# Kernel tuning notes

Measured on AMD Instinct MI355X. Metric: run time of the kernel, lower is better.

## Reference

```python
import jax, jax.numpy as jnp
import numpy as np

H = 64          # HIDDEN_DIM
V = 64          # VOCAB_SIZE
LN_EPS = 1e-5   # torch LayerNorm default
D_EPS = 1e-6    # denom epsilon in delta rule
MEM_SCALE = 1.0 # forward default arg


def setup_inputs() -> dict:
    key = jax.random.key(0)
    ks = jax.random.split(key, 8)
    B, L = 16, 2048
    s = lambda k, shape: (jax.random.normal(k, shape, jnp.float32) * 0.05)
    return {
        "seq": jax.random.randint(ks[0], (B, L), 0, V),
        "embed": s(ks[1], (V, H)),
        "W1": s(ks[2], (H, 2 * H)), "b1": jnp.zeros((2 * H,), jnp.float32),
        "W2": s(ks[3], (2 * H, H)), "b2": jnp.zeros((H,), jnp.float32),
        "gamma": jnp.ones((H,), jnp.float32), "beta": jnp.zeros((H,), jnp.float32),
        "Wr": s(ks[4], (H, H)), "br": jnp.zeros((H,), jnp.float32),
        "Wo": s(ks[5], (H, V)), "bo": jnp.zeros((V,), jnp.float32),
    }


def reference(seq, embed, W1, b1, W2, b2, gamma, beta, Wr, br, Wo, bo):
    h = embed[seq]                                  # (B, L, H)
    ff = jax.nn.relu(h @ W1 + b1) @ W2 + b2         # (B, L, H)
    x = h + ff
    mu = x.mean(-1, keepdims=True)
    var = x.var(-1, keepdims=True)                  # biased, as torch LayerNorm
    h = (x - mu) / jnp.sqrt(var + LN_EPS) * gamma + beta

    B = h.shape[0]
    keys = jnp.swapaxes(h[:, :-1, :], 0, 1)         # (L-1, B, H): all but last token

    def step(M, k):                                  # M: (B, H, H), k: (B, H)
        v_pred = jnp.einsum('bij,bj->bi', M, k)
        denom = (k * k).sum(-1, keepdims=True) + D_EPS
        dv = k - v_pred / denom
        M = M + MEM_SCALE * dv[:, :, None] * k[:, None, :]
        return M, None

    M0 = jnp.zeros((B, H, H), h.dtype)
    M, _ = jax.lax.scan(step, M0, keys)

    q = h[:, -1, :]                                  # last token as query
    ctx = jnp.einsum('bij,bj->bi', M, q)             # (B, H)
    return (ctx @ Wr + br) @ Wo + bo                 # (B, V)
```

## Files before the change

### kernel.cpp

```cpp
#include <hip/hip_runtime.h>

#define HDIM 64
#define LSEQ 2048
#define BATCH 16
#define LN_EPS 1e-5f
#define D_EPS 1e-6f
#define NSEG 32
#define CPS 4

typedef unsigned short u16;
typedef unsigned int   u32;
typedef __attribute__((ext_vector_type(8))) short bf16x8;
typedef __attribute__((ext_vector_type(4))) float f32x4;

__device__ __forceinline__ float bf2f(u16 v) {
    return __uint_as_float(((u32)v) << 16);
}
__device__ __forceinline__ u16 f2bf(float f) {
    u32 u = __float_as_uint(f);
    return (u16)((u + 0x7FFFu + ((u >> 16) & 1u)) >> 16);
}

#define A_W1F  0
#define A_W2F  16384
#define A_ER   32768
#define A_HF   50176
#define H_ROWS 66560
#define H_INVD 75264
#define SMEM_BYTES 75520
#define B_GM 0
#define B_BH 4352
#define B_BL 13568
#define B_SH 22784
#define B_SL 32000
#define B_ZN 41216
#define B_ZV 46336

__global__ __launch_bounds__(256, 2) void fused_pc_kernel(
    const int* __restrict__ seq, const float* __restrict__ embed,
    const float* __restrict__ W1, const float* __restrict__ b1,
    const float* __restrict__ W2, const float* __restrict__ b2,
    const float* __restrict__ gamma, const float* __restrict__ beta,
    u32* __restrict__ PK, u16* __restrict__ q_ws)
{
    __shared__ __align__(16) char smem[SMEM_BYTES];
    const int t = threadIdx.x;
    const int b = blockIdx.x >> 5;
    const int s = blockIdx.x & 31;
    const int tok0 = 1984 - 64 * s;

    u16*   hrows  = (u16*)(smem + H_ROWS);
    float* invd_l = (float*)(smem + H_INVD);

    const int lane = t & 63;
    const int w    = t >> 6;
    const int g    = lane >> 4;
    const int c    = lane & 15;

    {
        u16*   sW1f = (u16*)(smem + A_W1F);
        u16*   sW2f = (u16*)(smem + A_W2F);
        float* eR   = (float*)(smem + A_ER);
        u16*   hF   = (u16*)(smem + A_HF);

        {
            const float4* s1 = (const float4*)W1;
#pragma unroll
            for (int q = 0; q < 8; ++q) {
                const int m = t + 256 * q;
                const int k = m >> 5;
                const int o0 = (m & 31) * 4;
                const float4 v = s1[m];
                const float e4[4] = {v.x, v.y, v.z, v.w};
                const int ks = k >> 5, l4 = ((k >> 3) & 3) << 4, i = k & 7;
#pragma unroll
                for (int e = 0; e < 4; ++e) {
                    const int o = o0 + e;
                    sW1f[((ks * 8 + (o >> 4)) * 64 + l4 + (o & 15)) * 8 + i] = f2bf(e4[e]);
                }
            }
            const float4* s2 = (const float4*)W2;
#pragma unroll
            for (int q = 0; q < 8; ++q) {
                const int m = t + 256 * q;
                const int k = m >> 4;
                const int o0 = (m & 15) * 4;
                const float4 v = s2[m];
                const float e4[4] = {v.x, v.y, v.z, v.w};
                const int ks = k >> 5, l4 = ((k >> 3) & 3) << 4, i = k & 7;
#pragma unroll
                for (int e = 0; e < 4; ++e) {
                    const int o = o0 + e;
                    sW2f[((ks * 4 + (o >> 4)) * 64 + l4 + (o & 15)) * 8 + i] = f2bf(e4[e]);
                }
            }
        }
        {
            const int tk = t >> 2, p = t & 3;
            const int v = seq[b * LSEQ + tok0 + tk];
            const float* er = embed + v * HDIM + 16 * p;
#pragma unroll
            for (int q = 0; q < 4; ++q)
                *(float4*)&eR[tk * 68 + 16 * p + 4 * q] = *(const float4*)(er + 4 * q);
        }
        __syncthreads();

        bf16x8 ea[2];
#pragma unroll
        for (int ks = 0; ks < 2; ++ks) {
            const float* src = &eR[(16 * w + c) * 68 + ks * 32 + g * 8];
            const float4 v0 = *(const float4*)src;
            const float4 v1 = *(const float4*)(src + 4);
            bf16x8 f;
            f[0] = (short)f2bf(v0.x); f[1] = (short)f2bf(v0.y);
            f[2] = (short)f2bf(v0.z); f[3] = (short)f2bf(v0.w);
            f[4] = (short)f2bf(v1.x); f[5] = (short)f2bf(v1.y);
            f[6] = (short)f2bf(v1.z); f[7] = (short)f2bf(v1.w);
            ea[ks] = f;
        }

#pragma unroll
        for (int nt = 0; nt < 8; ++nt) {
            const float bv = b1[16 * nt + c];
            f32x4 acc = {bv, bv, bv, bv};
#pragma unroll
            for (int ks = 0; ks < 2; ++ks) {
                const bf16x8 bf = *(const bf16x8*)&sW1f[((ks * 8 + nt) * 64 + lane) * 8];
                acc = __builtin_amdgcn_mfma_f32_16x16x32_bf16(ea[ks], bf, acc, 0, 0, 0);
            }
            const int o   = 16 * nt + c;
            const int ks2 = o >> 5;
            const int l4  = ((o >> 3) & 3) << 4;
            const int i   = o & 7;
#pragma unroll
            for (int r = 0; r < 4; ++r) {
                const float hv = fmaxf(acc[r], 0.f);
                hF[((w * 4 + ks2) * 64 + l4 + g * 4 + r) * 8 + i] = f2bf(hv);
            }
        }

        bf16x8 ha[4];
#pragma unroll
        for (int ks = 0; ks < 4; ++ks)
            ha[ks] = *(const bf16x8*)&hF[((w * 4 + ks) * 64 + lane) * 8];

        float xf[4][4];
#pragma unroll
        for (int nt = 0; nt < 4; ++nt) {
            const float bv = b2[16 * nt + c];
            f32x4 acc = {bv, bv, bv, bv};
#pragma unroll
            for (int ks = 0; ks < 4; ++ks) {
                const bf16x8 bf = *(const bf16x8*)&sW2f[((ks * 4 + nt) * 64 + lane) * 8];
                acc = __builtin_amdgcn_mfma_f32_16x16x32_bf16(ha[ks], bf, acc, 0, 0, 0);
            }
#pragma unroll
            for (int r = 0; r < 4; ++r)
                xf[nt][r] = acc[r] + eR[(16 * w + g * 4 + r) * 68 + 16 * nt + c];
        }

        float s4[4] = {0, 0, 0, 0}, q4[4] = {0, 0, 0, 0};
#pragma unroll
        for (int nt = 0; nt < 4; ++nt)
#pragma unroll
            for (int r = 0; r < 4; ++r) {
                s4[r] += xf[nt][r];
                q4[r] = fmaf(xf[nt][r], xf[nt][r], q4[r]);
            }
#pragma unroll
        for (int m = 1; m < 16; m <<= 1)
#pragma unroll
            for (int r = 0; r < 4; ++r) {
                s4[r] += __shfl_xor(s4[r], m);
                q4[r] += __shfl_xor(q4[r], m);
            }
        float mu[4], rstd[4];
#pragma unroll
        for (int r = 0; r < 4; ++r) {
            mu[r] = s4[r] * (1.0f / 64.0f);
            const float var = q4[r] * (1.0f / 64.0f) - mu[r] * mu[r];
            rstd[r] = 1.0f / sqrtf(var + LN_EPS);
        }

        float hh[4] = {0, 0, 0, 0};
#pragma unroll
        for (int nt = 0; nt < 4; ++nt) {
            const int o = 16 * nt + c;
            const float gm = gamma[o], bt = beta[o];
#pragma unroll
            for (int r = 0; r < 4; ++r) {
                const float ov = (xf[nt][r] - mu[r]) * rstd[r] * gm + bt;
                const u16 rb = f2bf(ov);
                const float qf = bf2f(rb);
                hh[r] = fmaf(qf, qf, hh[r]);
                u16 st = rb;
                if (s == 0 && w == 3 && g == 3 && r == 3) {
                    q_ws[b * 64 + o] = rb;
                    st = 0;
                }
                hrows[(16 * w + g * 4 + r) * 68 + o] = st;
            }
        }
#pragma unroll
        for (int m = 1; m < 16; m <<= 1)
#pragma unroll
            for (int r = 0; r < 4; ++r) hh[r] += __shfl_xor(hh[r], m);
        if (c == 0) {
#pragma unroll
            for (int r = 0; r < 4; ++r)
                invd_l[16 * w + g * 4 + r] = 1.0f / (hh[r] + D_EPS);
        }
    }
    __syncthreads();

    {
        float* Gm = (float*)(smem + B_GM) + w * 272;
        u16*   Bh = (u16*)(smem + B_BH) + w * 1152;
        u16*   Bl = (u16*)(smem + B_BL) + w * 1152;
        u16*   Sh = (u16*)(smem + B_SH) + w * 1152;
        u16*   Sl = (u16*)(smem + B_SL) + w * 1152;
        u32*   Zn = (u32*)(smem + B_ZN) + w * 320;
        u32*   Zv = (u32*)(smem + B_ZV) + w * 320;

        f32x4 Sacc[4], Vacc[4];
#pragma unroll
        for (int mt = 0; mt < 4; ++mt) {
            ushort4 h4, l4;
            u16* hp = (u16*)&h4;
#pragma unroll
            for (int r = 0; r < 4; ++r) {
                const int m = 16 * mt + 4 * g + r;
                const float v = (m == 16 * w + c) ? 1.0f : 0.0f;
                Sacc[mt][r] = v;
                Vacc[mt][r] = 0.f;
                hp[r] = f2bf(v);
            }
            l4.x = 0; l4.y = 0; l4.z = 0; l4.w = 0;
            *(ushort4*)&Sh[c * 72 + 16 * mt + 4 * g] = h4;
            *(ushort4*)&Sl[c * 72 + 16 * mt + 4 * g] = l4;
        }

        for (int cc = 0; cc < CPS; ++cc) {
            const int base = 63 - 16 * cc;

            bf16x8 ka[2];
#pragma unroll
            for (int f = 0; f < 2; ++f) {
                const u16* src = &hrows[(base - c) * 68 + f * 32 + g * 8];
                const ushort4 a0 = *(const ushort4*)src;
                const ushort4 a1 = *(const ushort4*)(src + 4);
                bf16x8 kf;
                kf[0] = (short)a0.x; kf[1] = (short)a0.y; kf[2] = (short)a0.z; kf[3] = (short)a0.w;
                kf[4] = (short)a1.x; kf[5] = (short)a1.y; kf[6] = (short)a1.z; kf[7] = (short)a1.w;
                ka[f] = kf;
            }
            f32x4 gacc = {0.f, 0.f, 0.f, 0.f};
            gacc = __builtin_amdgcn_mfma_f32_16x16x32_bf16(ka[0], ka[0], gacc, 0, 0, 0);
            gacc = __builtin_amdgcn_mfma_f32_16x16x32_bf16(ka[1], ka[1], gacc, 0, 0, 0);
            const float ivc = invd_l[base - c];
#pragma unroll
            for (int r = 0; r < 4; ++r)
                Gm[(4 * g + r) * 17 + c] = gacc[r] * ivc;

            float Breg[16];
#pragma unroll
            for (int i = 0; i < 16; ++i) {
                float acc = bf2f(hrows[(base - i) * 68 + lane]);
#pragma unroll
                for (int j = 0; j < 16; ++j)
                    if (j < i) acc = fmaf(-Gm[i * 17 + j], Breg[j], acc);
                Breg[i] = acc;
            }
#pragma unroll
            for (int i = 0; i < 16; ++i) {
                const u16 hb = f2bf(Breg[i]);
                const u16 lb = f2bf(Breg[i] - bf2f(hb));
                Bh[i * 72 + lane] = hb;
                Bl[i * 72 + lane] = lb;
            }

            const bf16x8 abh0 = *(const bf16x8*)&Bh[c * 72 +  0 + g * 8];
            const bf16x8 abh1 = *(const bf16x8*)&Bh[c * 72 + 32 + g * 8];
            const bf16x8 abl0 = *(const bf16x8*)&Bl[c * 72 +  0 + g * 8];
            const bf16x8 abl1 = *(const bf16x8*)&Bl[c * 72 + 32 + g * 8];
            const bf16x8 sh0  = *(const bf16x8*)&Sh[c * 72 +  0 + g * 8];
            const bf16x8 sh1  = *(const bf16x8*)&Sh[c * 72 + 32 + g * 8];
            const bf16x8 sl0  = *(const bf16x8*)&Sl[c * 72 +  0 + g * 8];
            const bf16x8 sl1  = *(const bf16x8*)&Sl[c * 72 + 32 + g * 8];
            f32x4 zacc = {0.f, 0.f, 0.f, 0.f};
            zacc = __builtin_amdgcn_mfma_f32_16x16x32_bf16(abh0, sh0, zacc, 0, 0, 0);
            zacc = __builtin_amdgcn_mfma_f32_16x16x32_bf16(abh1, sh1, zacc, 0, 0, 0);
            zacc = __builtin_amdgcn_mfma_f32_16x16x32_bf16(abh0, sl0, zacc, 0, 0, 0);
            zacc = __builtin_amdgcn_mfma_f32_16x16x32_bf16(abh1, sl1, zacc, 0, 0, 0);
            zacc = __builtin_amdgcn_mfma_f32_16x16x32_bf16(abl0, sh0, zacc, 0, 0, 0);
            zacc = __builtin_amdgcn_mfma_f32_16x16x32_bf16(abl1, sh1, zacc, 0, 0, 0);

            uint4 znp, zvp;
            u32* znpp = (u32*)&znp;
            u32* zvpp = (u32*)&zvp;
#pragma unroll
            for (int r = 0; r < 4; ++r) {
                const int j = 4 * g + r;
                const float iv = invd_l[base - j];
                const float z  = zacc[r];
                const float zt = -z * iv;
                const u16 nh = f2bf(zt);
                const u16 nl = f2bf(zt - bf2f(nh));
                znpp[r] = ((u32)nh << 16) | (u32)nl;
                const u16 vh = f2bf(z);
                const u16 vl = f2bf(z - bf2f(vh));
                zvpp[r] = ((u32)vh << 16) | (u32)vl;
            }
            *(uint4*)&Zn[c * 20 + 4 * g] = znp;
            *(uint4*)&Zv[c * 20 + 4 * g] = zvp;

            const int j0 = (g & 1) * 8;
            const uint4 za0 = *(const uint4*)&Zn[c * 20 + j0];
            const uint4 za1 = *(const uint4*)&Zn[c * 20 + j0 + 4];
            const uint4 zb0 = *(const uint4*)&Zv[c * 20 + j0];
            const uint4 zb1 = *(const uint4*)&Zv[c * 20 + j0 + 4];
            bf16x8 znf, zvf;
            {
                const u32 zn8[8] = {za0.x, za0.y, za0.z, za0.w, za1.x, za1.y, za1.z, za1.w};
                const u32 zv8[8] = {zb0.x, zb0.y, zb0.z, zb0.w, zb1.x, zb1.y, zb1.z, zb1.w};
                const bool hi = (g < 2);
#pragma unroll
                for (int i8 = 0; i8 < 8; ++i8) {
                    znf[i8] = (short)(hi ? (zn8[i8] >> 16) : (zn8[i8] & 0xFFFFu));
                    zvf[i8] = (short)(hi ? (zv8[i8] >> 16) : (zv8[i8] & 0xFFFFu));
                }
            }

#pragma unroll
            for (int mt = 0; mt < 4; ++mt) {
                bf16x8 kaf;
#pragma unroll
                for (int i8 = 0; i8 < 8; ++i8)
                    kaf[i8] = (short)hrows[(base - (j0 + i8)) * 68 + 16 * mt + c];
                Sacc[mt] = __builtin_amdgcn_mfma_f32_16x16x32_bf16(kaf, znf, Sacc[mt], 0, 0, 0);
                Vacc[mt] = __builtin_amdgcn_mfma_f32_16x16x32_bf16(kaf, zvf, Vacc[mt], 0, 0, 0);
            }
            if (cc < CPS - 1) {
#pragma unroll
                for (int mt = 0; mt < 4; ++mt) {
                    ushort4 h4, l4;
                    u16* hp = (u16*)&h4;
                    u16* lp = (u16*)&l4;
#pragma unroll
                    for (int r = 0; r < 4; ++r) {
                        const float sv = Sacc[mt][r];
                        const u16 hb = f2bf(sv);
                        hp[r] = hb;
                        lp[r] = f2bf(sv - bf2f(hb));
                    }
                    *(ushort4*)&Sh[c * 72 + 16 * mt + 4 * g] = h4;
                    *(ushort4*)&Sl[c * 72 + 16 * mt + 4 * g] = l4;
                }
            }
        }

        u32* pk = PK + ((size_t)(b * NSEG + s) << 12);
#pragma unroll
        for (int mt = 0; mt < 4; ++mt) {
            uint4 o;
            u32* op = (u32*)&o;
#pragma unroll
            for (int r = 0; r < 4; ++r)
                op[r] = ((u32)f2bf(Sacc[mt][r]) << 16) | (u32)f2bf(Vacc[mt][r]);
            *(uint4*)&pk[(16 * w + c) * 64 + 16 * mt + 4 * g] = o;
        }
    }
}

__global__ __launch_bounds__(256, 1) void final_kernel(
    const u16* __restrict__ q_ws, const u32* __restrict__ PK,
    const float* __restrict__ Wr, const float* __restrict__ br,
    const float* __restrict__ Wo, const float* __restrict__ bo,
    float* __restrict__ out)
{
    const int b    = blockIdx.x;
    const int t    = threadIdx.x;
    const int lane = t & 63;
    const int p    = t >> 6;

    __shared__ float psum[4][72];
    __shared__ float rl[64];
    __shared__ float cs[64], rs[64];

    rl[lane] = bf2f(q_ws[b * 64 + lane]);

    float ctxp = 0.f;
    u32 cur[16], nxt[16];
    {
        const u32* pk0 = PK + ((size_t)(b * NSEG + 0) << 12);
#pragma unroll
        for (int jj = 0; jj < 16; ++jj)
            cur[jj] = pk0[(p * 16 + jj) * 64 + lane];
    }
    __syncthreads();

    for (int s = 0; s < NSEG; ++s) {
        const int sn = (s + 1 < NSEG) ? s + 1 : s;
        const u32* pkn = PK + ((size_t)(b * NSEG + sn) << 12);
#pragma unroll
        for (int jj = 0; jj < 16; ++jj)
            nxt[jj] = pkn[(p * 16 + jj) * 64 + lane];

        float accr = 0.f;
#pragma unroll
        for (int jj = 0; jj < 16; ++jj) {
            const u32 pv = cur[jj];
            const float Sv = __uint_as_float(pv & 0xFFFF0000u);
            const float Vv = __uint_as_float(pv << 16);
            const float rj = rl[p * 16 + jj];
            accr = fmaf(Sv, rj, accr);
            ctxp = fmaf(Vv, rj, ctxp);
        }
        psum[p][lane] = accr;
        __syncthreads();
        const float rn = (psum[0][lane] + psum[1][lane]) + (psum[2][lane] + psum[3][lane]);
        __syncthreads();
        rl[lane] = rn;

#pragma unroll
        for (int jj = 0; jj < 16; ++jj) cur[jj] = nxt[jj];
    }

    psum[p][lane] = ctxp;
    __syncthreads();
    if (t < 64)
        cs[t] = (psum[0][t] + psum[1][t]) + (psum[2][t] + psum[3][t]);
    __syncthreads();

    float rv = (p == 0) ? br[lane] : 0.f;
#pragma unroll
    for (int i = 0; i < 16; ++i)
        rv = fmaf(cs[p * 16 + i], Wr[(p * 16 + i) * HDIM + lane], rv);
    psum[p][lane] = rv;
    __syncthreads();
    if (t < 64)
        rs[t] = (psum[0][t] + psum[1][t]) + (psum[2][t] + psum[3][t]);
    __syncthreads();

    float ov = (p == 0) ? bo[lane] : 0.f;
#pragma unroll
    for (int i = 0; i < 16; ++i)
        ov = fmaf(rs[p * 16 + i], Wo[(p * 16 + i) * HDIM + lane], ov);
    psum[p][lane] = ov;
    __syncthreads();
    if (t < 64)
        out[(size_t)b * HDIM + t] = (psum[0][t] + psum[1][t]) + (psum[2][t] + psum[3][t]);
}

extern "C" void kernel_launch(void* const* d_in, const int* in_sizes, int n_in,
                              void* d_out, int out_size, void* d_ws, size_t ws_size,
                              hipStream_t stream)
{
    const int*   seq   = (const int*)  d_in[0];
    const float* embed = (const float*)d_in[1];
    const float* W1    = (const float*)d_in[2];
    const float* b1    = (const float*)d_in[3];
    const float* W2    = (const float*)d_in[4];
    const float* b2    = (const float*)d_in[5];
    const float* gamma = (const float*)d_in[6];
    const float* beta  = (const float*)d_in[7];
    const float* Wr    = (const float*)d_in[8];
    const float* br    = (const float*)d_in[9];
    const float* Wo    = (const float*)d_in[10];
    const float* bo    = (const float*)d_in[11];

    u32* pk_ws = (u32*)d_ws;
    u16* q_ws  = (u16*)(pk_ws + (size_t)BATCH * NSEG * 4096);
    float* outp = (float*)d_out;

    hipLaunchKernelGGL(fused_pc_kernel, dim3(BATCH * NSEG), dim3(256), 0, stream,
                       seq, embed, W1, b1, W2, b2, gamma, beta, pk_ws, q_ws);
    hipLaunchKernelGGL(final_kernel, dim3(BATCH), dim3(256), 0, stream,
                       q_ws, pk_ws, Wr, br, Wo, bo, outp);
}
```

Measured before the change: 119.7 us.

## Pre-pack FFN weights in separate kernel, shrink LDS, share chunk solve across waves

Result: faster. 114.1 us (-4.7%).

```diff
diff --git a/kernel.cpp b/kernel.cpp
--- a/kernel.cpp
+++ b/kernel.cpp
@@ -21,25 +21,50 @@
     return (u16)((u + 0x7FFFu + ((u >> 16) & 1u)) >> 16);
 }
 
-#define A_W1F  0
-#define A_W2F  16384
-#define A_ER   32768
-#define A_HF   50176
-#define H_ROWS 66560
-#define H_INVD 75264
-#define SMEM_BYTES 75520
-#define B_GM 0
-#define B_BH 4352
-#define B_BL 13568
-#define B_SH 22784
-#define B_SL 32000
-#define B_ZN 41216
-#define B_ZV 46336
-
-__global__ __launch_bounds__(256, 2) void fused_pc_kernel(
+#define A_ER   0
+#define A_HF   17408
+#define B_GM   0
+#define B_BH   1088
+#define B_BL   3392
+#define B_SH   5696
+#define B_SL   14912
+#define B_ZN   24128
+#define B_ZV   29248
+#define H_ROWS 34368
+#define H_T    43072
+#define H_INVD 52288
+#define SMEM_BYTES 52544
+
+__global__ __launch_bounds__(256) void prep_w_kernel(
+    const float* __restrict__ W1, const float* __restrict__ W2,
+    u16* __restrict__ W1F, u16* __restrict__ W2F)
+{
+    const int sIdx = blockIdx.x * 256 + threadIdx.x;
+    const int s10  = sIdx & 1023;
+    const int f    = s10 >> 6, l = s10 & 63;
+    const int cc   = l & 15,  gg = l >> 4;
+    u16 tmp[8];
+    if (sIdx < 1024) {
+        const int ks = f >> 3, nt = f & 7;
+        const int o = nt * 16 + cc, k0 = ks * 32 + gg * 8;
+#pragma unroll
+        for (int i = 0; i < 8; ++i) tmp[i] = f2bf(W1[(k0 + i) * 128 + o]);
+        *(ushort4*)&W1F[s10 * 8]     = *(ushort4*)&tmp[0];
+        *(ushort4*)&W1F[s10 * 8 + 4] = *(ushort4*)&tmp[4];
+    } else {
+        const int ks = f >> 2, nt = f & 3;
+        const int o = nt * 16 + cc, k0 = ks * 32 + gg * 8;
+#pragma unroll
+        for (int i = 0; i < 8; ++i) tmp[i] = f2bf(W2[(k0 + i) * 64 + o]);
+        *(ushort4*)&W2F[s10 * 8]     = *(ushort4*)&tmp[0];
+        *(ushort4*)&W2F[s10 * 8 + 4] = *(ushort4*)&tmp[4];
+    }
+}
+
+__global__ __launch_bounds__(256, 3) void fused_pc_kernel(
     const int* __restrict__ seq, const float* __restrict__ embed,
-    const float* __restrict__ W1, const float* __restrict__ b1,
-    const float* __restrict__ W2, const float* __restrict__ b2,
+    const u16* __restrict__ W1F, const float* __restrict__ b1,
+    const u16* __restrict__ W2F, const float* __restrict__ b2,
     const float* __restrict__ gamma, const float* __restrict__ beta,
     u32* __restrict__ PK, u16* __restrict__ q_ws)
 {
@@ -50,6 +75,7 @@
     const int tok0 = 1984 - 64 * s;
 
     u16*   hrows  = (u16*)(smem + H_ROWS);
+    u16*   hT     = (u16*)(smem + H_T);
     float* invd_l = (float*)(smem + H_INVD);
 
     const int lane = t & 63;
@@ -58,43 +84,9 @@
     const int c    = lane & 15;
 
     {
-        u16*   sW1f = (u16*)(smem + A_W1F);
-        u16*   sW2f = (u16*)(smem + A_W2F);
-        float* eR   = (float*)(smem + A_ER);
-        u16*   hF   = (u16*)(smem + A_HF);
-
-        {
-            const float4* s1 = (const float4*)W1;
-#pragma unroll
-            for (int q = 0; q < 8; ++q) {
-                const int m = t + 256 * q;
-                const int k = m >> 5;
-                const int o0 = (m & 31) * 4;
-                const float4 v = s1[m];
-                const float e4[4] = {v.x, v.y, v.z, v.w};
-                const int ks = k >> 5, l4 = ((k >> 3) & 3) << 4, i = k & 7;
-#pragma unroll
-                for (int e = 0; e < 4; ++e) {
-                    const int o = o0 + e;
-                    sW1f[((ks * 8 + (o >> 4)) * 64 + l4 + (o & 15)) * 8 + i] = f2bf(e4[e]);
-                }
-            }
-            const float4* s2 = (const float4*)W2;
-#pragma unroll
-            for (int q = 0; q < 8; ++q) {
-                const int m = t + 256 * q;
-                const int k = m >> 4;
-                const int o0 = (m & 15) * 4;
-                const float4 v = s2[m];
-                const float e4[4] = {v.x, v.y, v.z, v.w};
-                const int ks = k >> 5, l4 = ((k >> 3) & 3) << 4, i = k & 7;
-#pragma unroll
-                for (int e = 0; e < 4; ++e) {
-                    const int o = o0 + e;
-                    sW2f[((ks * 4 + (o >> 4)) * 64 + l4 + (o & 15)) * 8 + i] = f2bf(e4[e]);
-                }
-            }
-        }
+        float* eR = (float*)(smem + A_ER);
+        u16*   hF = (u16*)(smem + A_HF);
+
         {
             const int tk = t >> 2, p = t & 3;
             const int v = seq[b * LSEQ + tok0 + tk];
@@ -125,7 +117,7 @@
             f32x4 acc = {bv, bv, bv, bv};
 #pragma unroll
             for (int ks = 0; ks < 2; ++ks) {
-                const bf16x8 bf = *(const bf16x8*)&sW1f[((ks * 8 + nt) * 64 + lane) * 8];
+                const bf16x8 bf = *(const bf16x8*)&W1F[((ks * 8 + nt) * 64 + lane) * 8];
                 acc = __builtin_amdgcn_mfma_f32_16x16x32_bf16(ea[ks], bf, acc, 0, 0, 0);
             }
             const int o   = 16 * nt + c;
@@ -151,7 +143,7 @@
             f32x4 acc = {bv, bv, bv, bv};
 #pragma unroll
             for (int ks = 0; ks < 4; ++ks) {
-                const bf16x8 bf = *(const bf16x8*)&sW2f[((ks * 4 + nt) * 64 + lane) * 8];
+                const bf16x8 bf = *(const bf16x8*)&W2F[((ks * 4 + nt) * 64 + lane) * 8];
                 acc = __builtin_amdgcn_mfma_f32_16x16x32_bf16(ha[ks], bf, acc, 0, 0, 0);
             }
 #pragma unroll
@@ -198,7 +190,9 @@
                     q_ws[b * 64 + o] = rb;
                     st = 0;
                 }
-                hrows[(16 * w + g * 4 + r) * 68 + o] = st;
+                const int row = 16 * w + 4 * g + r;
+                hrows[row * 68 + o] = st;
+                hT[o * 72 + row]    = st;
             }
         }
 #pragma unroll
@@ -214,9 +208,9 @@
     __syncthreads();
 
     {
-        float* Gm = (float*)(smem + B_GM) + w * 272;
-        u16*   Bh = (u16*)(smem + B_BH) + w * 1152;
-        u16*   Bl = (u16*)(smem + B_BL) + w * 1152;
+        float* Gm = (float*)(smem + B_GM);
+        u16*   Bh = (u16*)(smem + B_BH);
+        u16*   Bl = (u16*)(smem + B_BL);
         u16*   Sh = (u16*)(smem + B_SH) + w * 1152;
         u16*   Sl = (u16*)(smem + B_SL) + w * 1152;
         u32*   Zn = (u32*)(smem + B_ZN) + w * 320;
@@ -240,13 +234,12 @@
             *(ushort4*)&Sl[c * 72 + 16 * mt + 4 * g] = l4;
         }
 
-        for (int cc = 0; cc < CPS; ++cc) {
-            const int base = 63 - 16 * cc;
-
+        if (w == 0) {
+            const int basep = 63;
             bf16x8 ka[2];
 #pragma unroll
             for (int f = 0; f < 2; ++f) {
-                const u16* src = &hrows[(base - c) * 68 + f * 32 + g * 8];
+                const u16* src = &hrows[(basep - c) * 68 + f * 32 + g * 8];
                 const ushort4 a0 = *(const ushort4*)src;
                 const ushort4 a1 = *(const ushort4*)(src + 4);
                 bf16x8 kf;
@@ -257,27 +250,42 @@
             f32x4 gacc = {0.f, 0.f, 0.f, 0.f};
             gacc = __builtin_amdgcn_mfma_f32_16x16x32_bf16(ka[0], ka[0], gacc, 0, 0, 0);
             gacc = __builtin_amdgcn_mfma_f32_16x16x32_bf16(ka[1], ka[1], gacc, 0, 0, 0);
-            const float ivc = invd_l[base - c];
+            const float ivc = invd_l[basep - c];
 #pragma unroll
             for (int r = 0; r < 4; ++r)
                 Gm[(4 * g + r) * 17 + c] = gacc[r] * ivc;
-
-            float Breg[16];
-#pragma unroll
-            for (int i = 0; i < 16; ++i) {
-                float acc = bf2f(hrows[(base - i) * 68 + lane]);
-#pragma unroll
-                for (int j = 0; j < 16; ++j)
-                    if (j < i) acc = fmaf(-Gm[i * 17 + j], Breg[j], acc);
-                Breg[i] = acc;
-            }
-#pragma unroll
-            for (int i = 0; i < 16; ++i) {
-                const u16 hb = f2bf(Breg[i]);
-                const u16 lb = f2bf(Breg[i] - bf2f(hb));
-                Bh[i * 72 + lane] = hb;
-                Bl[i * 72 + lane] = lb;
-            }
+        }
+
+        for (int cc = 0; cc < CPS; ++cc) {
+            const int base = 63 - 16 * cc;
+            __syncthreads();
+
+            if (g == 0) {
+                const int m = 16 * w + c;
+                const u16* hp = &hT[m * 72 + base - 15];
+                const ushort4 k0 = *(const ushort4*)&hp[0];
+                const ushort4 k1 = *(const ushort4*)&hp[4];
+                const ushort4 k2 = *(const ushort4*)&hp[8];
+                const ushort4 k3 = *(const ushort4*)&hp[12];
+                const u16 kv[16] = {k0.x, k0.y, k0.z, k0.w, k1.x, k1.y, k1.z, k1.w,
+                                    k2.x, k2.y, k2.z, k2.w, k3.x, k3.y, k3.z, k3.w};
+                float Breg[16];
+#pragma unroll
+                for (int i = 0; i < 16; ++i) {
+                    float acc = bf2f(kv[15 - i]);
+#pragma unroll
+                    for (int j = 0; j < 16; ++j)
+                        if (j < i) acc = fmaf(-Gm[i * 17 + j], Breg[j], acc);
+                    Breg[i] = acc;
+                }
+#pragma unroll
+                for (int i = 0; i < 16; ++i) {
+                    const u16 hb = f2bf(Breg[i]);
+                    Bh[i * 72 + m] = hb;
+                    Bl[i * 72 + m] = f2bf(Breg[i] - bf2f(hb));
+                }
+            }
+            __syncthreads();
 
             const bf16x8 abh0 = *(const bf16x8*)&Bh[c * 72 +  0 + g * 8];
             const bf16x8 abh1 = *(const bf16x8*)&Bh[c * 72 + 32 + g * 8];
@@ -333,10 +341,14 @@
 
 #pragma unroll
             for (int mt = 0; mt < 4; ++mt) {
+                const u16* kp = &hT[(16 * mt + c) * 72 + base - j0 - 7];
+                const ushort4 ta = *(const ushort4*)&kp[0];
+                const ushort4 tb = *(const ushort4*)&kp[4];
+                const u16 kvv[8] = {ta.x, ta.y, ta.z, ta.w, tb.x, tb.y, tb.z, tb.w};
                 bf16x8 kaf;
 #pragma unroll
                 for (int i8 = 0; i8 < 8; ++i8)
-                    kaf[i8] = (short)hrows[(base - (j0 + i8)) * 68 + 16 * mt + c];
+                    kaf[i8] = (short)kvv[7 - i8];
                 Sacc[mt] = __builtin_amdgcn_mfma_f32_16x16x32_bf16(kaf, znf, Sacc[mt], 0, 0, 0);
                 Vacc[mt] = __builtin_amdgcn_mfma_f32_16x16x32_bf16(kaf, zvf, Vacc[mt], 0, 0, 0);
             }
@@ -356,6 +368,27 @@
                     *(ushort4*)&Sh[c * 72 + 16 * mt + 4 * g] = h4;
                     *(ushort4*)&Sl[c * 72 + 16 * mt + 4 * g] = l4;
                 }
+            }
+            if (w == 0 && cc + 1 < CPS) {
+                const int basep = base - 16;
+                bf16x8 ka[2];
+#pragma unroll
+                for (int f = 0; f < 2; ++f) {
+                    const u16* src = &hrows[(basep - c) * 68 + f * 32 + g * 8];
+                    const ushort4 a0 = *(const ushort4*)src;
+                    const ushort4 a1 = *(const ushort4*)(src + 4);
+                    bf16x8 kf;
+                    kf[0] = (short)a0.x; kf[1] = (short)a0.y; kf[2] = (short)a0.z; kf[3] = (short)a0.w;
+                    kf[4] = (short)a1.x; kf[5] = (short)a1.y; kf[6] = (short)a1.z; kf[7] = (short)a1.w;
+                    ka[f] = kf;
+                }
+                f32x4 gacc = {0.f, 0.f, 0.f, 0.f};
+                gacc = __builtin_amdgcn_mfma_f32_16x16x32_bf16(ka[0], ka[0], gacc, 0, 0, 0);
+                gacc = __builtin_amdgcn_mfma_f32_16x16x32_bf16(ka[1], ka[1], gacc, 0, 0, 0);
+                const float ivc = invd_l[basep - c];
+#pragma unroll
+                for (int r = 0; r < 4; ++r)
+                    Gm[(4 * g + r) * 17 + c] = gacc[r] * ivc;
             }
         }
 
@@ -471,10 +504,14 @@
 
     u32* pk_ws = (u32*)d_ws;
     u16* q_ws  = (u16*)(pk_ws + (size_t)BATCH * NSEG * 4096);
+    u16* W1F   = q_ws + (size_t)BATCH * 64;
+    u16* W2F   = W1F + 64 * 128;
     float* outp = (float*)d_out;
 
+    hipLaunchKernelGGL(prep_w_kernel, dim3(8), dim3(256), 0, stream,
+                       W1, W2, W1F, W2F);
     hipLaunchKernelGGL(fused_pc_kernel, dim3(BATCH * NSEG), dim3(256), 0, stream,
-                       seq, embed, W1, b1, W2, b2, gamma, beta, pk_ws, q_ws);
+                       seq, embed, W1F, b1, W2F, b2, gamma, beta, pk_ws, q_ws);
     hipLaunchKernelGGL(final_kernel, dim3(BATCH), dim3(256), 0, stream,
                        q_ws, pk_ws, Wr, br, Wo, bo, outp);
 }
```
